# Performance work log

Hardware: AMD Instinct MI355X
Metric: run time of the kernel (lower is better)

Reference implementation:

```python
import jax, jax.numpy as jnp
import numpy as np
from jax import lax

C = 64
RED = 8
BN_EPS = 1e-5

def _conv1x1(x, W, b):
    # x: [N,C,H,W], W: [O,C] (1x1 conv kernel squeezed), b: [O]
    return jnp.einsum('nchw,oc->nohw', x, W) + b[None, :, None, None]

def _cross_attention(img, depth, Wq, bq, Wk, bk, Wv, bv, gamma):
    # img, depth: [N,C,H,W]; channel-channel attention (attn is [N,C,C])
    N, c, H, Wd = img.shape
    HW = H * Wd
    q = _conv1x1(img, Wq, bq).reshape(N, c, HW).astype(jnp.float32)
    k = _conv1x1(depth, Wk, bk).reshape(N, c, HW).astype(jnp.float32)
    v = _conv1x1(depth, Wv, bv).reshape(N, c, HW).astype(jnp.float32)
    attn = jax.nn.softmax(jnp.einsum('nci,ndi->ncd', q, k), axis=-1)  # [N,C,C]
    out = jnp.einsum('ncd,ndi->nci', attn, v).reshape(N, c, H, Wd).astype(img.dtype)
    return gamma * out + img

def _mlp(x, w1, b1, w2, b2):
    h = jax.nn.relu(x @ w1.T + b1)
    return h @ w2.T + b2

def _cbam(x, fc1_w, fc1_b, fc2_w, fc2_b, sa_w, sa_b):
    # x: [N,C,H,W]
    avg = x.mean(axis=(2, 3))          # [N,C]
    mx = x.max(axis=(2, 3))            # [N,C]
    ch = jax.nn.sigmoid(_mlp(avg, fc1_w, fc1_b, fc2_w, fc2_b)
                        + _mlp(mx, fc1_w, fc1_b, fc2_w, fc2_b))  # [N,C]
    x = x * ch[:, :, None, None]
    sp_in = jnp.stack([x.mean(axis=1), x.max(axis=1)], axis=1)   # [N,2,H,W]
    sp = lax.conv_general_dilated(sp_in, sa_w, (1, 1), 'SAME',
                                  dimension_numbers=('NCHW', 'OIHW', 'NCHW')) + sa_b[None, :, None, None]
    return x * jax.nn.sigmoid(sp)


def setup_inputs() -> dict:
    key = jax.random.key(0)
    ks = jax.random.split(key, 20)
    B, S, H, W = 2, 8, 128, 128
    s = 0.05
    d = {
        'img_feat': jax.random.normal(ks[0], (B, S, C, H, W), jnp.float32),
        'depth_feat': jax.random.normal(ks[1], (B, S, C, H, W), jnp.float32),
        # CrossAttention (shared module, used for both directions)
        'Wq': jax.random.normal(ks[2], (C, C), jnp.float32) * s,
        'bq': jax.random.normal(ks[3], (C,), jnp.float32) * s,
        'Wk': jax.random.normal(ks[4], (C, C), jnp.float32) * s,
        'bk': jax.random.normal(ks[5], (C,), jnp.float32) * s,
        'Wv': jax.random.normal(ks[6], (C, C), jnp.float32) * s,
        'bv': jax.random.normal(ks[7], (C,), jnp.float32) * s,
        'gamma': jax.random.normal(ks[8], (1,), jnp.float32) * 0.5,
        # fusion conv (3x3, 2C -> C) + BN (inference, running stats)
        'Wf': jax.random.normal(ks[9], (C, 2 * C, 3, 3), jnp.float32) * s,
        'bf': jax.random.normal(ks[10], (C,), jnp.float32) * s,
        'bn_g': jnp.ones((C,), jnp.float32),
        'bn_b': jnp.zeros((C,), jnp.float32),
        'bn_m': jax.random.normal(ks[11], (C,), jnp.float32) * s,
        'bn_v': jax.random.uniform(ks[12], (C,), jnp.float32, 0.5, 1.5),
        # CBAM channel MLP + spatial conv (7x7, 2 -> 1)
        'fc1_w': jax.random.normal(ks[13], (C // RED, C), jnp.float32) * s,
        'fc1_b': jax.random.normal(ks[14], (C // RED,), jnp.float32) * s,
        'fc2_w': jax.random.normal(ks[15], (C, C // RED), jnp.float32) * s,
        'fc2_b': jax.random.normal(ks[16], (C,), jnp.float32) * s,
        'sa_w': jax.random.normal(ks[17], (1, 2, 7, 7), jnp.float32) * s,
        'sa_b': jax.random.normal(ks[18], (1,), jnp.float32) * s,
    }
    return d


def reference(img_feat, depth_feat, Wq, bq, Wk, bk, Wv, bv, gamma,
              Wf, bf, bn_g, bn_b, bn_m, bn_v,
              fc1_w, fc1_b, fc2_w, fc2_b, sa_w, sa_b):
    B, S, c, H, W = img_feat.shape
    img = img_feat.reshape(-1, c, H, W)
    dep = depth_feat.reshape(-1, c, H, W)
    img_att = _cross_attention(img, dep, Wq, bq, Wk, bk, Wv, bv, gamma)
    dep_att = _cross_attention(dep, img, Wq, bq, Wk, bk, Wv, bv, gamma)
    fused = jnp.concatenate([img_att, dep_att], axis=1)  # [N,2C,H,W]
    fused = lax.conv_general_dilated(fused, Wf, (1, 1), 'SAME',
                                     dimension_numbers=('NCHW', 'OIHW', 'NCHW')) + bf[None, :, None, None]
    inv = bn_g * lax.rsqrt(bn_v + BN_EPS)
    fused = jax.nn.relu(fused * inv[None, :, None, None] + (bn_b - bn_m * inv)[None, :, None, None])
    fused = _cbam(fused, fc1_w, fc1_b, fc2_w, fc2_b, sa_w, sa_b)
    return fused.reshape(B, S, c, H, W)
```

## Files before the change

### kernel.cpp

```cpp
#include <hip/hip_runtime.h>
#include <math.h>


typedef __bf16 bf16_t;
typedef bf16_t bf16x8 __attribute__((ext_vector_type(8)));
typedef bf16_t bf16x4 __attribute__((ext_vector_type(4)));
typedef float  f32x4  __attribute__((ext_vector_type(4)));
typedef _Float16 f16_t;
typedef f16_t  f16x8  __attribute__((ext_vector_type(8)));

static constexpr int  CH  = 64;
static constexpr int  H   = 128;
static constexpr int  W   = 128;
static constexpr int  HW  = H * W;
static constexpr int  NI  = 16;
static constexpr int  NCK = 32;

static constexpr int W_WQ=0, W_BQ=4096, W_WK=4160, W_BK=8256, W_WV=8320, W_BV=12416,
  W_GAMMA=12480, W_WF=12481, W_BF=86209, W_BNG=86273, W_BNB=86337, W_BNM=86401,
  W_BNV=86465, W_FC1W=86529, W_FC1B=87041, W_FC2W=87049, W_FC2B=87561,
  W_SAW=87625, W_SAB=87723, W_TOTAL=87724;

static constexpr size_t OFF_GPART  = 0;
static constexpr size_t SZ_GPART   = (size_t)NI*NCK*4096*4;
static constexpr size_t OFF_SX     = OFF_GPART + SZ_GPART;
static constexpr size_t SZ_SXY     = (size_t)NI*NCK*64*4;
static constexpr size_t OFF_SY     = OFF_SX + SZ_SXY;
static constexpr size_t OFF_M1     = OFF_SY + SZ_SXY;
static constexpr size_t SZ_M       = (size_t)NI*4096*4;
static constexpr size_t OFF_M2     = OFF_M1 + SZ_M;
static constexpr size_t OFF_T1     = OFF_M2 + SZ_M;
static constexpr size_t SZ_T       = (size_t)NI*64*4;
static constexpr size_t OFF_T2     = OFF_T1 + SZ_T;
static constexpr size_t OFF_BCONST = OFF_T2 + SZ_T;
static constexpr size_t OFF_WH     = OFF_BCONST + 256;
static constexpr size_t SZ_WH      = (size_t)NI*64*9*128*2;
static constexpr size_t OFF_WINDT  = OFF_WH + SZ_WH;
static constexpr size_t SZ_WIND    = (size_t)NI*9*64*4;
static constexpr size_t OFF_IND    = OFF_WINDT + SZ_WIND;
static constexpr size_t OFF_BSUM   = OFF_IND + SZ_WIND;
static constexpr size_t SZ_BST     = (size_t)NI*64*64*4;
static constexpr size_t OFF_BMAX   = OFF_BSUM + SZ_BST;
static constexpr size_t OFF_CHS    = OFF_BMAX + SZ_BST;
static constexpr size_t OFF_SPIN   = OFF_CHS + SZ_T;
static constexpr size_t SZ_SPIN    = (size_t)NI*2*HW*4;
static constexpr size_t OFF_FLAG   = OFF_SPIN + SZ_SPIN;
static constexpr size_t OFF_WF32   = OFF_FLAG + 256;
static constexpr size_t OFF_WFT    = ((OFF_WF32 + (size_t)W_TOTAL*4 + 255) / 256) * 256;
static constexpr size_t SZ_WFT     = (size_t)9*8192*4;
static constexpr size_t OFF_P16    = ((OFF_WFT + SZ_WFT + 255) / 256) * 256;
static constexpr size_t SZ_P16     = (size_t)NI*4*HW*32*2;

__global__ __launch_bounds__(256) void k0_detect(
    const unsigned short* __restrict__ u, int* __restrict__ flag)
{
  __shared__ int bad;
  if (threadIdx.x == 0) bad = 0;
  __syncthreads();
  int local = 0;
  for (int i = threadIdx.x; i < 4096; i += 256) {
    const unsigned short v = u[2*i];
    const int e = (v >> 7) & 0xFF;
    if (e >= 0xC0) local = 1;
  }
  if (local) atomicOr(&bad, 1);
  __syncthreads();
  if (threadIdx.x == 0) flag[0] = bad;
}

struct WPack { const void* p[19]; int sz[19]; int off[19]; };

__global__ __launch_bounds__(256) void kwc_prep(
    WPack wp, const int* __restrict__ flag, float* __restrict__ dst,
    float* __restrict__ WFT,
    const bf16_t* __restrict__ Xb, const bf16_t* __restrict__ Yb,
    const float* __restrict__ Xf, const float* __restrict__ Yf,
    f16_t* __restrict__ P16, const int useP16)
{
  const int b = blockIdx.x;
  const int f32m = flag[0];
  if (b < 16384) {
    if (!useP16) return;
    const int lin = b * 256 + threadIdx.x;
    const int oct = lin & 3;
    const int p   = (lin >> 2) & 16383;
    const int s   = (lin >> 16) & 3;
    const int n   = lin >> 18;
    const size_t nbase = (size_t)n * CH * HW;
    const int c0 = (s & 1) * 32 + oct * 8;
    const float*  Fsrc = (s < 2) ? Xf : Yf;
    const bf16_t* Bsrc = (s < 2) ? Xb : Yb;
    f16x8 h;
    #pragma unroll
    for (int j = 0; j < 8; ++j) {
      const size_t q = nbase + (size_t)(c0 + j) * HW + p;
      const float v = f32m ? Fsrc[q] : (float)Bsrc[q];
      h[j] = (f16_t)v;
    }
    *(f16x8*)(P16 + (size_t)lin * 8) = h;
  } else {
    const int bb = b - 16384;
    const int j  = bb / 288;
    const int bx = bb % 288;
    const int i = bx * 256 + threadIdx.x;
    if (i >= wp.sz[j]) return;
    float v;
    if (f32m) v = ((const float*)wp.p[j])[i];
    else      v = (float)((const bf16_t*)wp.p[j])[i];
    dst[wp.off[j] + i] = v;
    if (j == 7) WFT[(i % 9) * 8192 + (i / 9)] = v;
  }
}

__global__ __launch_bounds__(256) void k1_gram(
    const bf16_t* __restrict__ Xb, const bf16_t* __restrict__ Yb,
    const float* __restrict__ Xf, const float* __restrict__ Yf,
    const int* __restrict__ flag,
    float* __restrict__ Gpart, float* __restrict__ sxpart, float* __restrict__ sypart)
{
  const int chunk = blockIdx.x, n = blockIdx.y;
  const int t = threadIdx.x, lane = t & 63, wv = t >> 6;
  const int mrow = lane & 15, quad = lane >> 4;
  const int f32m = flag[0];
  const size_t nbase = (size_t)n * CH * HW;
  const int p0 = chunk * 512 + wv * 128;

  f32x4 acc[4][4], acc2[4][4];
  #pragma unroll
  for (int i = 0; i < 4; ++i)
    #pragma unroll
    for (int j = 0; j < 4; ++j) {
      acc[i][j]  = (f32x4){0.f, 0.f, 0.f, 0.f};
      acc2[i][j] = (f32x4){0.f, 0.f, 0.f, 0.f};
    }
  float sxl[4] = {0.f,0.f,0.f,0.f}, syl[4] = {0.f,0.f,0.f,0.f};

  for (int kt = 0; kt < 4; ++kt) {
    const int pk = p0 + kt * 32 + quad * 8;
    if (f32m) {
      bf16x8 a[4], b[4], al[4], bl[4];
      #pragma unroll
      for (int mt = 0; mt < 4; ++mt) {
        const size_t ia = nbase + (size_t)(mt*16 + mrow) * HW + pk;
        float sa = 0.f, sb = 0.f;
        #pragma unroll
        for (int j = 0; j < 8; ++j) {
          const float va = Xf[ia + j];
          const bf16_t ha = (bf16_t)va;
          a[mt][j] = ha; al[mt][j] = (bf16_t)(va - (float)ha); sa += va;
          const float vb = Yf[ia + j];
          const bf16_t hb = (bf16_t)vb;
          b[mt][j] = hb; bl[mt][j] = (bf16_t)(vb - (float)hb); sb += vb;
        }
        sxl[mt] += sa; syl[mt] += sb;
      }
      #pragma unroll
      for (int mt = 0; mt < 4; ++mt)
        #pragma unroll
        for (int nt = 0; nt < 4; ++nt) {
          acc[mt][nt]  = __builtin_amdgcn_mfma_f32_16x16x32_bf16(a[mt],  b[nt],  acc[mt][nt],  0, 0, 0);
          acc2[mt][nt] = __builtin_amdgcn_mfma_f32_16x16x32_bf16(a[mt],  bl[nt], acc2[mt][nt], 0, 0, 0);
          acc2[mt][nt] = __builtin_amdgcn_mfma_f32_16x16x32_bf16(al[mt], b[nt],  acc2[mt][nt], 0, 0, 0);
        }
    } else {
      bf16x8 a[4], b[4];
      #pragma unroll
      for (int mt = 0; mt < 4; ++mt) {
        const size_t ia = nbase + (size_t)(mt*16 + mrow) * HW + pk;
        a[mt] = *(const bf16x8*)(Xb + ia);
        b[mt] = *(const bf16x8*)(Yb + ia);
        float sa = 0.f, sb = 0.f;
        #pragma unroll
        for (int j = 0; j < 8; ++j) { sa += (float)a[mt][j]; sb += (float)b[mt][j]; }
        sxl[mt] += sa; syl[mt] += sb;
      }
      #pragma unroll
      for (int mt = 0; mt < 4; ++mt)
        #pragma unroll
        for (int nt = 0; nt < 4; ++nt)
          acc[mt][nt] = __builtin_amdgcn_mfma_f32_16x16x32_bf16(a[mt], b[nt], acc[mt][nt], 0, 0, 0);
    }
  }

  #pragma unroll
  for (int mt = 0; mt < 4; ++mt) {
    sxl[mt] += __shfl_xor(sxl[mt], 16, 64); sxl[mt] += __shfl_xor(sxl[mt], 32, 64);
    syl[mt] += __shfl_xor(syl[mt], 16, 64); syl[mt] += __shfl_xor(syl[mt], 32, 64);
  }

  __shared__ float Gs[4096];
  __shared__ float sxs[64], sys[64];
  for (int w2 = 0; w2 < 4; ++w2) {
    if (wv == w2) {
      #pragma unroll
      for (int mt = 0; mt < 4; ++mt) {
        #pragma unroll
        for (int nt = 0; nt < 4; ++nt) {
          #pragma unroll
          for (int r = 0; r < 4; ++r) {
            const int c = mt*16 + quad*4 + r, d = nt*16 + mrow;
            const float val = acc[mt][nt][r] + acc2[mt][nt][r];
            if (w2 == 0) Gs[c*64 + d]  = val;
            else         Gs[c*64 + d] += val;
          }
        }
        if (quad == 0) {
          const int c = mt*16 + mrow;
          if (w2 == 0) { sxs[c] = sxl[mt];  sys[c] = syl[mt]; }
          else         { sxs[c] += sxl[mt]; sys[c] += syl[mt]; }
        }
      }
    }
    __syncthreads();
  }
  float* Gp = Gpart + ((size_t)n*NCK + chunk) * 4096;
  for (int i = t; i < 4096; i += 256) Gp[i] = Gs[i];
  if (t < 64)       sxpart[((size_t)n*NCK + chunk)*64 + t]        = sxs[t];
  else if (t < 128) sypart[((size_t)n*NCK + chunk)*64 + (t - 64)] = sys[t - 64];
}

__global__ __launch_bounds__(256, 1) void k2a_attn(
    const float* __restrict__ Gpart, const float* __restrict__ sxpart, const float* __restrict__ sypart,
    const float* __restrict__ wt,
    float* __restrict__ M1, float* __restrict__ M2,
    float* __restrict__ T1, float* __restrict__ T2)
{
  const int bx = blockIdx.x, n = blockIdx.y;
  const int dir  = bx & 1;
  const int c0   = (bx >> 1) * 32;
  const int t = threadIdx.x;
  constexpr int SW = 68;
  __shared__ float Gs[4096];
  __shared__ float Ps[4096];
  __shared__ float As[64*SW];
  __shared__ float WQs[64*SW], WKs[64*SW], WVs[64*SW];
  __shared__ float sxs[64], sys[64], uu[64], vv[64];

  for (int i = t; i < 4096; i += 256) {
    const int r = i >> 6, cc = i & 63;
    WQs[r*SW + cc] = wt[W_WQ + i];
    WKs[r*SW + cc] = wt[W_WK + i];
    WVs[r*SW + cc] = wt[W_WV + i];
  }
  for (int i4 = t; i4 < 1024; i4 += 256) {
    f32x4 s = (f32x4){0.f, 0.f, 0.f, 0.f};
    for (int c2 = 0; c2 < NCK; ++c2)
      s += *(const f32x4*)(Gpart + ((size_t)n*NCK + c2)*4096 + i4*4);
    *(f32x4*)(Gs + i4*4) = s;
  }
  if (t < 64) {
    float s = 0.f; for (int c2 = 0; c2 < NCK; ++c2) s += sxpart[((size_t)n*NCK + c2)*64 + t];
    sxs[t] = s;
  } else if (t < 128) {
    const int c = t - 64;
    float s = 0.f; for (int c2 = 0; c2 < NCK; ++c2) s += sypart[((size_t)n*NCK + c2)*64 + c];
    sys[c] = s;
  }
  __syncthreads();

  {
    const int e = t & 63;
    float Greg[64];
    if (dir == 0) {
      #pragma unroll
      for (int a = 0; a < 64; ++a) Greg[a] = Gs[a*64 + e];
    } else {
      #pragma unroll
      for (int a4 = 0; a4 < 16; ++a4)
        *(f32x4*)(Greg + a4*4) = *(const f32x4*)(Gs + e*64 + a4*4);
    }
    for (int it = 0; it < 8; ++it) {
      const int c = c0 + (t >> 6) + 4*it;
      float s1 = 0.f;
      #pragma unroll
      for (int a4 = 0; a4 < 16; ++a4) {
        const f32x4 w4 = *(const f32x4*)(WQs + c*SW + a4*4);
        #pragma unroll
        for (int r = 0; r < 4; ++r) s1 += w4[r] * Greg[a4*4 + r];
      }
      Ps[c*64 + e] = s1;
    }
  }
  {
    const int c = t & 63;
    if (t < 64) {
      const float* vecv = dir ? sys : sxs;
      float s = 0.f;
      #pragma unroll
      for (int a = 0; a < 64; ++a) s += WQs[c*SW + a] * vecv[a];
      uu[c] = s;
    } else if (t < 128) {
      const float* vecv = dir ? sxs : sys;
      float s = 0.f;
      #pragma unroll
      for (int a = 0; a < 64; ++a) s += WKs[c*SW + a] * vecv[a];
      vv[c] = s;
    }
  }
  __syncthreads();

  {
    const int d = t & 63;
    float WKreg[64];
    #pragma unroll
    for (int a4 = 0; a4 < 16; ++a4)
      *(f32x4*)(WKreg + a4*4) = *(const f32x4*)(WKs + d*SW + a4*4);
    const float bkd = wt[W_BK + d];
    for (int it = 0; it < 8; ++it) {
      const int c = c0 + (t >> 6) + 4*it;
      float s1 = 0.f;
      #pragma unroll
      for (int e4 = 0; e4 < 16; ++e4) {
        const f32x4 p1 = *(const f32x4*)(Ps + c*64 + e4*4);
        #pragma unroll
        for (int r = 0; r < 4; ++r) s1 += p1[r] * WKreg[e4*4 + r];
      }
      const float bqc = wt[W_BQ + c];
      s1 += uu[c]*bkd + bqc*vv[d] + 16384.f*bqc*bkd;
      As[c*SW + d] = s1;
    }
  }
  __syncthreads();

  if (t < 32) {
    float* R = As + (c0 + t)*SW;
    float m = R[0];
    for (int d = 1; d < 64; ++d) m = fmaxf(m, R[d]);
    float s = 0.f;
    for (int d = 0; d < 64; ++d) { const float e2 = expf(R[d] - m); R[d] = e2; s += e2; }
    const float inv = 1.f / s;
    for (int d = 0; d < 64; ++d) R[d] *= inv;
  }
  __syncthreads();

  {
    const int e = t & 63;
    float WVreg[64];
    #pragma unroll
    for (int dd = 0; dd < 64; ++dd) WVreg[dd] = WVs[dd*SW + e];
    float* Mo = (dir ? M2 : M1) + (size_t)n*4096;
    for (int it = 0; it < 8; ++it) {
      const int c = c0 + (t >> 6) + 4*it;
      float s1 = 0.f;
      #pragma unroll
      for (int d4 = 0; d4 < 16; ++d4) {
        const f32x4 a1 = *(const f32x4*)(As + c*SW + d4*4);
        #pragma unroll
        for (int r = 0; r < 4; ++r) s1 += a1[r] * WVreg[d4*4 + r];
      }
      Mo[c*64 + e] = s1;
    }
  }
  if (t < 32) {
    const int c = c0 + t;
    float s1 = 0.f;
    for (int d = 0; d < 64; ++d) s1 += As[c*SW + d] * wt[W_BV + d];
    (dir ? T2 : T1)[n*64 + c] = s1;
  }
}

__global__ __launch_bounds__(256) void k2b_weff(
    const float* __restrict__ wt, const float* __restrict__ WFT,
    const float* __restrict__ M1, const float* __restrict__ M2,
    const float* __restrict__ T1, const float* __restrict__ T2,
    f16_t* __restrict__ Wh, float* __restrict__ windT, float* __restrict__ bconst)
{
  const int tap = blockIdx.x, dir = blockIdx.y, n = blockIdx.z;
  const int t = threadIdx.x;
  const float g = wt[W_GAMMA];
  f16_t* Whn = Wh + (size_t)n * 64 * 9 * 128;
  const float* Mo = (dir == 0) ? (M2 + (size_t)n*4096) : (M1 + (size_t)n*4096);

  __shared__ float Wfs[8192];
  __shared__ float Ms[4096];

  for (int i4 = t; i4 < 2048; i4 += 256)
    *(f32x4*)(Wfs + i4*4) = *(const f32x4*)(WFT + (size_t)tap*8192 + i4*4);
  for (int i4 = t; i4 < 1024; i4 += 256)
    *(f32x4*)(Ms + i4*4) = *(const f32x4*)(Mo + i4*4);
  __syncthreads();

  const int e = t & 63;
  float Msreg[64];
  #pragma unroll
  for (int c = 0; c < 64; ++c) Msreg[c] = Ms[c*64 + e];
  const int coff = dir ? 0 : 64;
  const int boff = dir ? 64 : 0;
  for (int it = 0; it < 16; ++it) {
    const int o = (t >> 6) + 4*it;
    const float inv = wt[W_BNG + o] * rsqrtf(wt[W_BNV + o] + 1e-5f);
    const float base = Wfs[o*128 + boff + e];
    float s = 0.f;
    #pragma unroll
    for (int c4 = 0; c4 < 16; ++c4) {
      const f32x4 w4 = *(const f32x4*)(Wfs + o*128 + coff + c4*4);
      #pragma unroll
      for (int r = 0; r < 4; ++r) s += w4[r] * Msreg[c4*4 + r];
    }
    Whn[(o*9 + tap)*128 + dir*64 + e] = (f16_t)(inv * (base + g * s));
  }

  if (dir == 0 && t < 64) {
    const int o = t;
    const float inv = wt[W_BNG + o] * rsqrtf(wt[W_BNV + o] + 1e-5f);
    float s = 0.f;
    for (int c = 0; c < 64; ++c)
      s += wt[W_WF + (o*128 + c)*9 + tap]      * T1[n*64 + c]
         + wt[W_WF + (o*128 + 64 + c)*9 + tap] * T2[n*64 + c];
    windT[((size_t)n*9 + tap)*64 + o] = inv * g * s;
    if (tap == 0 && n == 0)
      bconst[o] = wt[W_BF + o]*inv + wt[W_BNB + o] - wt[W_BNM + o]*inv;
  }
}

__global__ __launch_bounds__(512) void k3_conv(
    const bf16_t* __restrict__ Xb, const bf16_t* __restrict__ Yb,
    const float* __restrict__ Xf, const float* __restrict__ Yf,
    const int* __restrict__ flag,
    const f16_t* __restrict__ Wh, const float* __restrict__ bconst,
    const float* __restrict__ windT,
    const f16_t* __restrict__ P16, const int useP16,
    bf16_t* __restrict__ fusedB, float* __restrict__ fusedF,
    float* __restrict__ bsum, float* __restrict__ bmax)
{
  __shared__ __attribute__((aligned(16))) f16_t sbuf[6][130][40];
  __shared__ float sind[576], sconst[64];
  __shared__ float ssum[8][64], smax[8][64];
  const int rp = blockIdx.x, n = blockIdx.y;
  const int t = threadIdx.x, lane = t & 63, wv = t >> 6;
  const int l15 = lane & 15, quad = lane >> 4;
  const int ly = wv >> 1, ch2 = wv & 1;
  const int f32m = flag[0];
  const size_t nbase = (size_t)n * CH * HW;
  const f16_t* __restrict__ Whn = Wh + (size_t)n * 64 * 9 * 128;

  for (int i = t; i < 576; i += 512) {
    const int g = i >> 6, o = i & 63;
    const int yc = g / 3, xc = g % 3;
    const int ky0 = (yc == 0) ? 1 : 0, ky1 = (yc == 2) ? 1 : 2;
    const int kx0 = (xc == 0) ? 1 : 0, kx1 = (xc == 2) ? 1 : 2;
    float sv = 0.f;
    for (int ky = ky0; ky <= ky1; ++ky)
      for (int kx = kx0; kx <= kx1; ++kx)
        sv += windT[((size_t)n*9 + ky*3 + kx)*64 + o];
    sind[i] = sv;
  }
  if (t < 64) sconst[t] = bconst[t];
  if (t < 384) {
    const int r = t >> 6, cs = (t >> 5) & 1, sl = t & 31;
    sbuf[r][cs ? 129 : 0][sl] = (f16_t)0.f;
  }

  f32x4 acc[4][4];
  #pragma unroll
  for (int i = 0; i < 4; ++i)
    #pragma unroll
    for (int j = 0; j < 4; ++j) acc[i][j] = (f32x4){0.f, 0.f, 0.f, 0.f};

  if (useP16) {
    const int oct = t & 3;
    const int x   = t >> 2;
    const f16_t* __restrict__ PnB = P16 + (size_t)(n*4) * HW * 32;
    f16x8 h[6];

    #define K3_STAGE_LOAD(S)                                                  \
      { const f16_t* __restrict__ Pn = PnB + (size_t)(S) * HW * 32;           \
        _Pragma("unroll")                                                     \
        for (int i = 0; i < 6; ++i) {                                         \
          const int gy = rp*4 - 1 + i;                                        \
          f16x8 v;                                                            \
          _Pragma("unroll")                                                   \
          for (int k2 = 0; k2 < 8; ++k2) v[k2] = (f16_t)0.f;                  \
          if (gy >= 0 && gy < H)                                              \
            v = *(const f16x8*)(Pn + ((size_t)(gy*128 + x) * 32 + oct*8));    \
          h[i] = v;                                                           \
        } }
    #define K3_STAGE_WRITE()                                                  \
      { const int colL = x + 1;                                               \
        _Pragma("unroll")                                                     \
        for (int i = 0; i < 6; ++i)                                           \
          *(f16x8*)&sbuf[i][colL][(oct ^ (colL & 3)) * 8] = h[i];             \
      }

    K3_STAGE_LOAD(0)
    K3_STAGE_WRITE()
    for (int s = 0; s < 4; ++s) {
      if (s < 3) K3_STAGE_LOAD(s + 1)
      asm volatile("s_waitcnt lgkmcnt(0)" ::: "memory");
      __builtin_amdgcn_s_barrier();
      __builtin_amdgcn_s_setprio(1);
      #pragma unroll
      for (int tap = 0; tap < 9; ++tap) {
        const int ky = tap / 3, kx = tap % 3;
        f16x8 bfr[4];
        #pragma unroll
        for (int nt = 0; nt < 4; ++nt) {
          const int o = nt*16 + l15;
          bfr[nt] = *(const f16x8*)(Whn + ((o*9 + tap)*128 + s*32 + quad*8));
        }
        f16x8 afr[4];
        const int row = ly + ky;
        #pragma unroll
        for (int mt = 0; mt < 4; ++mt) {
          const int col = ch2*64 + mt*16 + l15 + kx;
          afr[mt] = *(const f16x8*)&sbuf[row][col][(quad ^ (col & 3)) * 8];
        }
        #pragma unroll
        for (int mt = 0; mt < 4; ++mt)
          #pragma unroll
          for (int nt = 0; nt < 4; ++nt)
            acc[mt][nt] = __builtin_amdgcn_mfma_f32_16x16x32_f16(afr[mt], bfr[nt], acc[mt][nt], 0, 0, 0);
      }
      __builtin_amdgcn_s_setprio(0);
      __builtin_amdgcn_s_barrier();
      if (s < 3) K3_STAGE_WRITE()
    }
    #undef K3_STAGE_LOAD
    #undef K3_STAGE_WRITE
  } else {
    const int cstage = t & 127, rsel = t >> 7;
    for (int s = 0; s < 4; ++s) {
      __syncthreads();
      #pragma unroll
      for (int pass = 0; pass < 2; ++pass) {
        const int r = rsel + 4*pass;
        if (r < 6) {
          const int gy = rp*4 - 1 + r;
          const bool valid = (gy >= 0) && (gy < H);
          const int colL = cstage + 1;
          #pragma unroll
          for (int oct = 0; oct < 4; ++oct) {
            f16x8 hh;
            #pragma unroll
            for (int j = 0; j < 8; ++j) {
              const int g = s*32 + oct*8 + j;
              float v = 0.f;
              if (valid) {
                const size_t q = nbase + (size_t)(g & 63)*HW + gy*W + cstage;
                v = (g < 64) ? (f32m ? Xf[q] : (float)Xb[q])
                             : (f32m ? Yf[q] : (float)Yb[q]);
              }
              hh[j] = (f16_t)v;
            }
            *(f16x8*)&sbuf[r][colL][(oct ^ (colL & 3)) * 8] = hh;
          }
        }
      }
      __syncthreads();
      #pragma unroll
      for (int tap = 0; tap < 9; ++tap) {
        const int ky = tap / 3, kx = tap % 3;
        f16x8 bfr[4];
        #pragma unroll
        for (int nt = 0; nt < 4; ++nt) {
          const int o = nt*16 + l15;
          bfr[nt] = *(const f16x8*)(Whn + ((o*9 + tap)*128 + s*32 + quad*8));
        }
        f16x8 afr[4];
        const int row = ly + ky;
        #pragma unroll
        for (int mt = 0; mt < 4; ++mt) {
          const int col = ch2*64 + mt*16 + l15 + kx;
          afr[mt] = *(const f16x8*)&sbuf[row][col][(quad ^ (col & 3)) * 8];
        }
        #pragma unroll
        for (int mt = 0; mt < 4; ++mt)
          #pragma unroll
          for (int nt = 0; nt < 4; ++nt)
            acc[mt][nt] = __builtin_amdgcn_mfma_f32_16x16x32_f16(afr[mt], bfr[nt], acc[mt][nt], 0, 0, 0);
      }
    }
  }

  const int y = rp*4 + ly;
  const int yc = (y == 0) ? 0 : (y == H-1) ? 2 : 1;
  #pragma unroll
  for (int nt = 0; nt < 4; ++nt) {
    const int o = nt*16 + l15;
    const float bc = sconst[o];
    float ssm = 0.f, smx = 0.f;
    #pragma unroll
    for (int mt = 0; mt < 4; ++mt) {
      const int xb = ch2*64 + mt*16 + quad*4;
      f32x4 vals;
      #pragma unroll
      for (int r = 0; r < 4; ++r) {
        const int x = xb + r;
        const int xc = (x == 0) ? 0 : (x == W-1) ? 2 : 1;
        float v = acc[mt][nt][r] + bc + sind[(yc*3 + xc)*64 + o];
        v = fmaxf(v, 0.f);
        vals[r] = v; ssm += v; smx = fmaxf(smx, v);
      }
      const size_t off = nbase + (size_t)o*HW + y*W + xb;
      if (f32m) {
        *(f32x4*)(fusedF + off) = vals;
      } else {
        bf16x4 pv;
        #pragma unroll
        for (int r = 0; r < 4; ++r) pv[r] = (bf16_t)vals[r];
        *(bf16x4*)(fusedB + off) = pv;
      }
    }
    ssm += __shfl_xor(ssm, 16, 64); ssm += __shfl_xor(ssm, 32, 64);
    smx = fmaxf(smx, __shfl_xor(smx, 16, 64));
    smx = fmaxf(smx, __shfl_xor(smx, 32, 64));
    if (quad == 0) { ssum[wv][o] = ssm; smax[wv][o] = smx; }
  }
  __syncthreads();
  if (t < 64) {
    float S = 0.f, M = 0.f;
    #pragma unroll
    for (int w2 = 0; w2 < 8; ++w2) {
      S += ssum[w2][t];
      M = fmaxf(M, smax[w2][t]);
    }
    bsum[((size_t)n*32 + rp)*64 + t] = S;
    bmax[((size_t)n*32 + rp)*64 + t] = M;
  }
}

__global__ __launch_bounds__(256) void k4_chgate(
    const float* __restrict__ bsum, const float* __restrict__ bmax,
    const float* __restrict__ wt, float* __restrict__ chout)
{
  const int n = blockIdx.x, t = threadIdx.x;
  const int o = t & 63, part = t >> 6;
  __shared__ float ps[4][64], pm[4][64];
  __shared__ float avg[64], mxs[64], h1[8], h2[8];
  float S = 0.f, M = 0.f;
  for (int rp = part*8; rp < part*8 + 8; ++rp) {
    S += bsum[((size_t)n*32 + rp)*64 + o];
    M = fmaxf(M, bmax[((size_t)n*32 + rp)*64 + o]);
  }
  ps[part][o] = S; pm[part][o] = M;
  __syncthreads();
  if (t < 64) {
    const float Sa = ((ps[0][t] + ps[1][t]) + ps[2][t]) + ps[3][t];
    const float Ma = fmaxf(fmaxf(pm[0][t], pm[1][t]), fmaxf(pm[2][t], pm[3][t]));
    avg[t] = Sa * (1.f / 16384.f);
    mxs[t] = Ma;
  }
  __syncthreads();
  if (t < 8) {
    float s = wt[W_FC1B + t];
    for (int c = 0; c < 64; ++c) s += wt[W_FC1W + t*64 + c] * avg[c];
    h1[t] = fmaxf(s, 0.f);
  } else if (t < 16) {
    const int r = t - 8;
    float s = wt[W_FC1B + r];
    for (int c = 0; c < 64; ++c) s += wt[W_FC1W + r*64 + c] * mxs[c];
    h2[r] = fmaxf(s, 0.f);
  }
  __syncthreads();
  if (t < 64) {
    float s = 2.f * wt[W_FC2B + t];
    for (int r = 0; r < 8; ++r) s += wt[W_FC2W + t*8 + r] * (h1[r] + h2[r]);
    chout[n*64 + t] = 1.f / (1.f + expf(-s));
  }
}

__global__ __launch_bounds__(128) void k5_spin(
    const bf16_t* __restrict__ fusedB, const float* __restrict__ fusedF,
    const int* __restrict__ flag,
    const float* __restrict__ chs, float* __restrict__ spin)
{
  const int n = blockIdx.y;
  const int p0 = (blockIdx.x * 128 + threadIdx.x) * 8;
  const int f32m = flag[0];
  const size_t nbase = (size_t)n * CH * HW;
  const float* c = chs + n * 64;
  float s[8], m[8];
  #pragma unroll
  for (int k = 0; k < 8; ++k) { s[k] = 0.f; m[k] = 0.f; }
  if (f32m) {
    for (int o = 0; o < 64; ++o) {
      const float co = c[o];
      const float* q = fusedF + nbase + (size_t)o*HW + p0;
      const f32x4 a = *(const f32x4*)q;
      const f32x4 b = *(const f32x4*)(q + 4);
      #pragma unroll
      for (int k = 0; k < 4; ++k) {
        const float v0 = a[k] * co; s[k]   += v0; m[k]   = fmaxf(m[k],   v0);
        const float v1 = b[k] * co; s[4+k] += v1; m[4+k] = fmaxf(m[4+k], v1);
      }
    }
  } else {
    for (int o = 0; o < 64; ++o) {
      const float co = c[o];
      const bf16x8 a = *(const bf16x8*)(fusedB + nbase + (size_t)o*HW + p0);
      #pragma unroll
      for (int k = 0; k < 8; ++k) {
        const float v = (float)a[k] * co; s[k] += v; m[k] = fmaxf(m[k], v);
      }
    }
  }
  f32x4 o0, o1, o2, o3;
  #pragma unroll
  for (int k = 0; k < 4; ++k) {
    o0[k] = s[k]   * (1.f / 64.f);
    o1[k] = s[4+k] * (1.f / 64.f);
    o2[k] = m[k];
    o3[k] = m[4+k];
  }
  *(f32x4*)(spin + (size_t)n*2*HW + p0)          = o0;
  *(f32x4*)(spin + (size_t)n*2*HW + p0 + 4)      = o1;
  *(f32x4*)(spin + (size_t)n*2*HW + HW + p0)     = o2;
  *(f32x4*)(spin + (size_t)n*2*HW + HW + p0 + 4) = o3;
}

__global__ __launch_bounds__(128) void k6_final(
    bf16_t* __restrict__ fusedB, float* __restrict__ fusedF,
    const int* __restrict__ flag,
    const float* __restrict__ chs, const float* __restrict__ spin,
    const float* __restrict__ wt)
{
  const int n = blockIdx.y;
  const int p0 = (blockIdx.x * 128 + threadIdx.x) * 8;
  const int y = p0 >> 7, x0 = p0 & 127;
  const int f32m = flag[0];
  const float* s0 = spin + (size_t)n*2*HW;
  const float* s1 = s0 + HW;
  float acc[8];
  {
    const float sab = wt[W_SAB];
    #pragma unroll
    for (int k = 0; k < 8; ++k) acc[k] = sab;
  }
  for (int j = 0; j < 7; ++j) {
    const int yy = y + j - 3;
    if (yy < 0 || yy >= H) continue;
    const float* r0 = s0 + yy*W;
    const float* r1 = s1 + yy*W;
    float v0[14], v1[14];
    #pragma unroll
    for (int ii = 0; ii < 14; ++ii) {
      const int xx = x0 + ii - 3;
      const bool ok = (xx >= 0) && (xx < W);
      v0[ii] = ok ? r0[xx] : 0.f;
      v1[ii] = ok ? r1[xx] : 0.f;
    }
    #pragma unroll
    for (int i = 0; i < 7; ++i) {
      const float w0 = wt[W_SAW + j*7 + i];
      const float w1 = wt[W_SAW + 49 + j*7 + i];
      #pragma unroll
      for (int k = 0; k < 8; ++k)
        acc[k] += w0 * v0[i+k] + w1 * v1[i+k];
    }
  }
  float sp[8];
  #pragma unroll
  for (int k = 0; k < 8; ++k) sp[k] = 1.f / (1.f + expf(-acc[k]));
  const size_t nbase = (size_t)n * CH * HW;
  const float* c = chs + n * 64;
  if (f32m) {
    for (int o = 0; o < 64; ++o) {
      const float co = c[o];
      float* q = fusedF + nbase + (size_t)o*HW + p0;
      f32x4 a = *(f32x4*)q;
      f32x4 b = *(f32x4*)(q + 4);
      #pragma unroll
      for (int k = 0; k < 4; ++k) {
        a[k] = a[k] * co * sp[k];
        b[k] = b[k] * co * sp[4+k];
      }
      *(f32x4*)q       = a;
      *(f32x4*)(q + 4) = b;
    }
  } else {
    for (int o = 0; o < 64; ++o) {
      const float co = c[o];
      bf16_t* q = fusedB + nbase + (size_t)o*HW + p0;
      bf16x8 a = *(bf16x8*)q;
      #pragma unroll
      for (int k = 0; k < 8; ++k)
        a[k] = (bf16_t)((float)a[k] * co * sp[k]);
      *(bf16x8*)q = a;
    }
  }
}

extern "C" void kernel_launch(void* const* d_in, const int* in_sizes, int n_in,
                              void* d_out, int out_size, void* d_ws, size_t ws_size,
                              hipStream_t stream)
{
  (void)n_in; (void)out_size; (void)in_sizes;
  char* ws = (char*)d_ws;
  float*  Gpart  = (float*)(ws + OFF_GPART);
  float*  sxp    = (float*)(ws + OFF_SX);
  float*  syp    = (float*)(ws + OFF_SY);
  float*  M1     = (float*)(ws + OFF_M1);
  float*  M2     = (float*)(ws + OFF_M2);
  float*  T1     = (float*)(ws + OFF_T1);
  float*  T2     = (float*)(ws + OFF_T2);
  float*  bconst = (float*)(ws + OFF_BCONST);
  f16_t*  Wh     = (f16_t*)(ws + OFF_WH);
  float*  windT  = (float*)(ws + OFF_WINDT);
  float*  bsum   = (float*)(ws + OFF_BSUM);
  float*  bmax   = (float*)(ws + OFF_BMAX);
  float*  chs    = (float*)(ws + OFF_CHS);
  float*  spin   = (float*)(ws + OFF_SPIN);
  int*    flag   = (int*)  (ws + OFF_FLAG);
  float*  wf32   = (float*)(ws + OFF_WF32);
  float*  wft    = (float*)(ws + OFF_WFT);
  f16_t*  P16    = (f16_t*)(ws + OFF_P16);
  bf16_t* fusedB = (bf16_t*)d_out;
  float*  fusedF = (float*)d_out;

  const int useP16 = (ws_size >= OFF_P16 + SZ_P16) ? 1 : 0;

  const bf16_t* imgB = (const bf16_t*)d_in[0];
  const bf16_t* depB = (const bf16_t*)d_in[1];
  const float*  imgF = (const float*) d_in[0];
  const float*  depF = (const float*) d_in[1];

  WPack wp;
  static const int wsz[19] = {4096,64,4096,64,4096,64,1,73728,64,64,64,64,64,512,8,512,64,98,1};
  static const int woff[19] = {W_WQ,W_BQ,W_WK,W_BK,W_WV,W_BV,W_GAMMA,W_WF,W_BF,W_BNG,
                               W_BNB,W_BNM,W_BNV,W_FC1W,W_FC1B,W_FC2W,W_FC2B,W_SAW,W_SAB};
  for (int j = 0; j < 19; ++j) { wp.p[j] = d_in[2 + j]; wp.sz[j] = wsz[j]; wp.off[j] = woff[j]; }

  hipLaunchKernelGGL(k0_detect, dim3(1), dim3(256), 0, stream,
                     (const unsigned short*)d_in[0], flag);
  hipLaunchKernelGGL(kwc_prep, dim3(16384 + 5472), dim3(256), 0, stream,
                     wp, flag, wf32, wft, imgB, depB, imgF, depF, P16, useP16);
  hipLaunchKernelGGL(k1_gram,  dim3(NCK, NI), dim3(256), 0, stream,
                     imgB, depB, imgF, depF, flag, Gpart, sxp, syp);
  hipLaunchKernelGGL(k2a_attn, dim3(4, NI), dim3(256), 0, stream,
                     Gpart, sxp, syp, wf32, M1, M2, T1, T2);
  hipLaunchKernelGGL(k2b_weff, dim3(9, 2, NI), dim3(256), 0, stream,
                     wf32, wft, M1, M2, T1, T2, Wh, windT, bconst);
  hipLaunchKernelGGL(k3_conv,  dim3(32, NI), dim3(512), 0, stream,
                     imgB, depB, imgF, depF, flag, Wh, bconst, windT,
                     P16, useP16, fusedB, fusedF, bsum, bmax);
  hipLaunchKernelGGL(k4_chgate, dim3(NI), dim3(256), 0, stream,
                     bsum, bmax, wf32, chs);
  hipLaunchKernelGGL(k5_spin,  dim3(16, NI), dim3(128), 0, stream,
                     fusedB, fusedF, flag, chs, spin);
  hipLaunchKernelGGL(k6_final, dim3(16, NI), dim3(128), 0, stream,
                     fusedB, fusedF, flag, chs, spin, wf32);
}
```

Before: 424.8 us.

## Split channel reduction across waves and tile spatial conv through LDS

k5_spin now splits the 64-channel reduction across four waves per block and combines the partial sums and maxima through shared memory. This doubles the grid and raises the number of concurrent loads per pixel. k6_final stages a 10-row halo of the pooled maps in LDS, computes the 7x7 spatial conv two pixels per thread, and then spreads channels across waves for the final scaling pass. The aim is more parallelism and occupancy for these bandwidth-bound tail kernels, at the cost of extra LDS traffic and block barriers.

```diff
diff --git a/kernel.cpp b/kernel.cpp
--- a/kernel.cpp
+++ b/kernel.cpp
@@ -659,23 +659,27 @@
   }
 }
 
-__global__ __launch_bounds__(128) void k5_spin(
+__global__ __launch_bounds__(256) void k5_spin(
     const bf16_t* __restrict__ fusedB, const float* __restrict__ fusedF,
     const int* __restrict__ flag,
     const float* __restrict__ chs, float* __restrict__ spin)
 {
   const int n = blockIdx.y;
-  const int p0 = (blockIdx.x * 128 + threadIdx.x) * 8;
+  const int t = threadIdx.x, w = t >> 6, lane = t & 63;
+  const int px0 = blockIdx.x * 512 + lane * 8;
   const int f32m = flag[0];
   const size_t nbase = (size_t)n * CH * HW;
   const float* c = chs + n * 64;
+  __shared__ float Ssum[4][64][9], Smax[4][64][9];
   float s[8], m[8];
   #pragma unroll
   for (int k = 0; k < 8; ++k) { s[k] = 0.f; m[k] = 0.f; }
+  const int o0 = w * 16;
   if (f32m) {
-    for (int o = 0; o < 64; ++o) {
+    for (int oi = 0; oi < 16; ++oi) {
+      const int o = o0 + oi;
       const float co = c[o];
-      const float* q = fusedF + nbase + (size_t)o*HW + p0;
+      const float* q = fusedF + nbase + (size_t)o*HW + px0;
       const f32x4 a = *(const f32x4*)q;
       const f32x4 b = *(const f32x4*)(q + 4);
       #pragma unroll
@@ -685,77 +689,93 @@
       }
     }
   } else {
-    for (int o = 0; o < 64; ++o) {
+    for (int oi = 0; oi < 16; ++oi) {
+      const int o = o0 + oi;
       const float co = c[o];
-      const bf16x8 a = *(const bf16x8*)(fusedB + nbase + (size_t)o*HW + p0);
+      const bf16x8 a = *(const bf16x8*)(fusedB + nbase + (size_t)o*HW + px0);
       #pragma unroll
       for (int k = 0; k < 8; ++k) {
         const float v = (float)a[k] * co; s[k] += v; m[k] = fmaxf(m[k], v);
       }
     }
   }
-  f32x4 o0, o1, o2, o3;
   #pragma unroll
-  for (int k = 0; k < 4; ++k) {
-    o0[k] = s[k]   * (1.f / 64.f);
-    o1[k] = s[4+k] * (1.f / 64.f);
-    o2[k] = m[k];
-    o3[k] = m[4+k];
-  }
-  *(f32x4*)(spin + (size_t)n*2*HW + p0)          = o0;
-  *(f32x4*)(spin + (size_t)n*2*HW + p0 + 4)      = o1;
-  *(f32x4*)(spin + (size_t)n*2*HW + HW + p0)     = o2;
-  *(f32x4*)(spin + (size_t)n*2*HW + HW + p0 + 4) = o3;
-}
-
-__global__ __launch_bounds__(128) void k6_final(
+  for (int k = 0; k < 8; ++k) { Ssum[w][lane][k] = s[k]; Smax[w][lane][k] = m[k]; }
+  __syncthreads();
+  if (t < 64) {
+    const int p0 = blockIdx.x * 512 + t * 8;
+    f32x4 o0v, o1v, o2v, o3v;
+    #pragma unroll
+    for (int k = 0; k < 8; ++k) {
+      const float S = ((Ssum[0][t][k] + Ssum[1][t][k]) + Ssum[2][t][k]) + Ssum[3][t][k];
+      const float M = fmaxf(fmaxf(Smax[0][t][k], Smax[1][t][k]),
+                            fmaxf(Smax[2][t][k], Smax[3][t][k]));
+      if (k < 4) { o0v[k] = S * (1.f/64.f); o2v[k] = M; }
+      else       { o1v[k-4] = S * (1.f/64.f); o3v[k-4] = M; }
+    }
+    *(f32x4*)(spin + (size_t)n*2*HW + p0)          = o0v;
+    *(f32x4*)(spin + (size_t)n*2*HW + p0 + 4)      = o1v;
+    *(f32x4*)(spin + (size_t)n*2*HW + HW + p0)     = o2v;
+    *(f32x4*)(spin + (size_t)n*2*HW + HW + p0 + 4) = o3v;
+  }
+}
+
+__global__ __launch_bounds__(256) void k6_final(
     bf16_t* __restrict__ fusedB, float* __restrict__ fusedF,
     const int* __restrict__ flag,
     const float* __restrict__ chs, const float* __restrict__ spin,
     const float* __restrict__ wt)
 {
   const int n = blockIdx.y;
-  const int p0 = (blockIdx.x * 128 + threadIdx.x) * 8;
-  const int y = p0 >> 7, x0 = p0 & 127;
+  const int t = threadIdx.x;
+  const int y0 = blockIdx.x * 4;
   const int f32m = flag[0];
   const float* s0 = spin + (size_t)n*2*HW;
   const float* s1 = s0 + HW;
-  float acc[8];
-  {
-    const float sab = wt[W_SAB];
-    #pragma unroll
-    for (int k = 0; k < 8; ++k) acc[k] = sab;
-  }
-  for (int j = 0; j < 7; ++j) {
-    const int yy = y + j - 3;
-    if (yy < 0 || yy >= H) continue;
-    const float* r0 = s0 + yy*W;
-    const float* r1 = s1 + yy*W;
-    float v0[14], v1[14];
-    #pragma unroll
-    for (int ii = 0; ii < 14; ++ii) {
-      const int xx = x0 + ii - 3;
-      const bool ok = (xx >= 0) && (xx < W);
-      v0[ii] = ok ? r0[xx] : 0.f;
-      v1[ii] = ok ? r1[xx] : 0.f;
-    }
-    #pragma unroll
-    for (int i = 0; i < 7; ++i) {
-      const float w0 = wt[W_SAW + j*7 + i];
-      const float w1 = wt[W_SAW + 49 + j*7 + i];
-      #pragma unroll
-      for (int k = 0; k < 8; ++k)
-        acc[k] += w0 * v0[i+k] + w1 * v1[i+k];
-    }
-  }
+  __shared__ float s0l[10][128], s1l[10][128];
+  __shared__ float spl[8][64];
+
+  for (int i = t; i < 1280; i += 256) {
+    const int r = i >> 7, x = i & 127;
+    const int yy = y0 - 3 + r;
+    const bool ok = (yy >= 0) && (yy < H);
+    s0l[r][x] = ok ? s0[yy*W + x] : 0.f;
+    s1l[r][x] = ok ? s1[yy*W + x] : 0.f;
+  }
+  __syncthreads();
+
+  #pragma unroll
+  for (int pp = 0; pp < 2; ++pp) {
+    const int pl = t*2 + pp;
+    const int ly = pl >> 7, x = pl & 127;
+    float acc = wt[W_SAB];
+    #pragma unroll
+    for (int j = 0; j < 7; ++j) {
+      const int row = ly + j;
+      #pragma unroll
+      for (int i = 0; i < 7; ++i) {
+        const int xx = x + i - 3;
+        const bool ok = (xx >= 0) && (xx < W);
+        const float v0 = ok ? s0l[row][xx] : 0.f;
+        const float v1 = ok ? s1l[row][xx] : 0.f;
+        acc += wt[W_SAW + j*7 + i] * v0 + wt[W_SAW + 49 + j*7 + i] * v1;
+      }
+    }
+    spl[pl & 7][pl >> 3] = 1.f / (1.f + expf(-acc));
+  }
+  __syncthreads();
+
+  const size_t nbase = (size_t)n * CH * HW;
+  const float* c = chs + n * 64;
+  const int g = t & 63;
+  const int p0 = y0*W + g*8;
   float sp[8];
   #pragma unroll
-  for (int k = 0; k < 8; ++k) sp[k] = 1.f / (1.f + expf(-acc[k]));
-  const size_t nbase = (size_t)n * CH * HW;
-  const float* c = chs + n * 64;
-  if (f32m) {
-    for (int o = 0; o < 64; ++o) {
-      const float co = c[o];
+  for (int k = 0; k < 8; ++k) sp[k] = spl[k][g];
+  for (int it = 0; it < 16; ++it) {
+    const int o = it*4 + (t >> 6);
+    const float co = c[o];
+    if (f32m) {
       float* q = fusedF + nbase + (size_t)o*HW + p0;
       f32x4 a = *(f32x4*)q;
       f32x4 b = *(f32x4*)(q + 4);
@@ -766,10 +786,7 @@
       }
       *(f32x4*)q       = a;
       *(f32x4*)(q + 4) = b;
-    }
-  } else {
-    for (int o = 0; o < 64; ++o) {
-      const float co = c[o];
+    } else {
       bf16_t* q = fusedB + nbase + (size_t)o*HW + p0;
       bf16x8 a = *(bf16x8*)q;
       #pragma unroll
@@ -835,8 +852,8 @@
                      P16, useP16, fusedB, fusedF, bsum, bmax);
   hipLaunchKernelGGL(k4_chgate, dim3(NI), dim3(256), 0, stream,
                      bsum, bmax, wf32, chs);
-  hipLaunchKernelGGL(k5_spin,  dim3(16, NI), dim3(128), 0, stream,
+  hipLaunchKernelGGL(k5_spin,  dim3(32, NI), dim3(256), 0, stream,
                      fusedB, fusedF, flag, chs, spin);
-  hipLaunchKernelGGL(k6_final, dim3(16, NI), dim3(128), 0, stream,
+  hipLaunchKernelGGL(k6_final, dim3(32, NI), dim3(256), 0, stream,
                      fusedB, fusedF, flag, chs, spin, wf32);
 }
```

After: 422.0 us. About the same (-0.7%).
